# Kernel optimization log

Measured on AMD Instinct MI355X. Metric: run time of the kernel, lower is better.

The kernel has to match this reference:

```python
import jax, jax.numpy as jnp
import numpy as np

N_SAMPLES = 32768
N_FRAMES = 128
MODEL_DIM = 128
N_HARM = 64
N_EVENTS = 8
NYQ = 22050.0 / 2.0
MIN_F = 30.0 / NYQ
MAX_F = 3000.0 / NYQ
SPAN = MAX_F - MIN_F
PI = float(np.pi)


def linterp(x, size):
    # F.interpolate(mode='linear', align_corners=False) along last axis
    n_in = x.shape[-1]
    scale = n_in / size
    coords = (jnp.arange(size, dtype=jnp.float32) + 0.5) * scale - 0.5
    coords = jnp.clip(coords, 0.0, n_in - 1)
    lo = jnp.floor(coords).astype(jnp.int32)
    hi = jnp.minimum(lo + 1, n_in - 1)
    w = coords - lo.astype(jnp.float32)
    return x[..., lo] * (1.0 - w) + x[..., hi] * w


def gumbel_hard(logits, u):
    # F.gumbel_softmax(hard=True), straight-through, tau=1, last axis
    g = -jnp.log(-jnp.log(u + 1e-10) + 1e-10)
    y = jax.nn.softmax(logits + g, axis=-1)
    hard = jax.nn.one_hot(jnp.argmax(y, axis=-1), logits.shape[-1], dtype=y.dtype)
    return hard + y - jax.lax.stop_gradient(y)


def max_norm(x):
    return x / (jnp.max(jnp.abs(x), axis=-1, keepdims=True) + 1e-8)


def fft_convolve(a, b):
    sa = jnp.fft.rfft(a, axis=-1)
    sb = jnp.fft.rfft(b, axis=-1)
    return jnp.fft.irfft(sa * sb, n=a.shape[-1], axis=-1)


def setup_inputs() -> dict:
    key = jax.random.key(0)
    ks = jax.random.split(key, 16)
    B = 4 * N_EVENTS  # 32 flattened event vectors
    s = 0.1  # weight_init
    return {
        "x": jax.random.normal(ks[0], (B, MODEL_DIM), jnp.float32),
        "W_sw": jax.random.normal(ks[1], (MODEL_DIM, 2), jnp.float32) * s,
        "b_sw": jnp.zeros((2,), jnp.float32),
        "W_f0": jax.random.normal(ks[2], (MODEL_DIM, 1), jnp.float32) * s,
        "b_f0": jnp.zeros((1,), jnp.float32),
        "W_fv": jax.random.normal(ks[3], (MODEL_DIM, N_FRAMES), jnp.float32) * s,
        "b_fv": jnp.zeros((N_FRAMES,), jnp.float32),
        "W_amp": jax.random.normal(ks[4], (MODEL_DIM, 2 * N_HARM * N_FRAMES), jnp.float32) * s,
        "b_amp": jnp.zeros((2 * N_HARM * N_FRAMES,), jnp.float32),
        "W_loc": jax.random.normal(ks[5], (MODEL_DIM, N_FRAMES), jnp.float32) * s,
        "b_loc": jnp.zeros((N_FRAMES,), jnp.float32),
        "u_sw": jax.random.uniform(ks[6], (B, 2), jnp.float32),
        "u_loc": jax.random.uniform(ks[7], (B, 1, N_FRAMES), jnp.float32),
        "noise_u": jax.random.uniform(ks[8], (B, 1, N_SAMPLES), jnp.float32),
    }


def reference(x, W_sw, b_sw, W_f0, b_f0, W_fv, b_fv, W_amp, b_amp, W_loc, b_loc, u_sw, u_loc, noise_u):
    B = x.shape[0]
    # switch gate (gumbel hard), keep first channel
    sw = gumbel_hard(x @ W_sw + b_sw, u_sw)[..., :1]  # [B,1]
    # discrete location logits -> gumbel hard one-hot over 128 frames
    disc = jax.nn.sigmoid((x @ W_loc + b_loc).reshape(B, 1, N_FRAMES))
    loc = gumbel_hard(disc, u_loc).reshape(-1, N_EVENTS, N_FRAMES)  # [G,8,128]
    f0 = jax.nn.sigmoid(x @ W_f0 + b_f0) ** 2  # [B,1]
    f0_var = jax.nn.sigmoid((x @ W_fv + b_fv).reshape(B, 1, N_FRAMES)) * 2.0 - 1.0
    amp = ((x @ W_amp + b_amp).reshape(B, 2 * N_HARM, N_FRAMES)) ** 2
    # scatter one-hot locations onto full-rate timeline with stride
    step = N_SAMPLES // N_FRAMES
    loc_full = jnp.zeros((B // N_EVENTS, N_EVENTS, N_SAMPLES), x.dtype).at[:, :, ::step].set(loc)
    f0 = MIN_F + f0 * SPAN
    f0_span = f0 * 0.01
    f0t = f0.reshape(B, 1, 1) + f0_var * f0_span.reshape(B, 1, 1)  # [B,1,128]
    harmonics = jnp.arange(1, N_HARM + 1, dtype=x.dtype)
    harm = f0t * harmonics[None, :, None]  # [B,64,128]
    harm = jnp.where(harm > 1.0, 0.0, harm) * PI  # zero aliased harmonics
    harm = linterp(harm, N_SAMPLES)  # [B,64,N]
    harm = jnp.sin(jnp.cumsum(harm, axis=-1))  # phase-accumulated oscillators
    # noise shaped by 128-tap windowed slice of each oscillator
    noise = noise_u * 2.0 - 1.0  # uniform(-1,1), [B,1,N]
    hw = 0.54 - 0.46 * jnp.cos(2.0 * PI * jnp.arange(128, dtype=x.dtype) / 128.0)
    nf = harm[..., :128] * hw[None, None, :]
    nf = jnp.pad(nf, ((0, 0), (0, 0), (0, N_SAMPLES - 128)))
    nb = jnp.fft.irfft(jnp.fft.rfft(noise, axis=-1, norm='ortho') * jnp.fft.rfft(nf, axis=-1, norm='ortho'), n=N_SAMPLES, axis=-1, norm='ortho')
    nb = max_norm(nb)
    full = jnp.concatenate([harm, nb], axis=1)  # [B,128,N]
    amp = linterp(amp, N_SAMPLES)  # [B,128,N]
    out = full * amp * sw[..., None]
    out = out.reshape(-1, N_EVENTS, 2 * N_HARM, N_SAMPLES).sum(axis=2)  # [G,8,N]
    return fft_convolve(out, loc_full)
```

## Files before the change

### kernel.cpp

```cpp
#include <hip/hip_runtime.h>
#include <math.h>

typedef __attribute__((ext_vector_type(8))) short short8v;
typedef __attribute__((ext_vector_type(4))) float f32x4;

namespace {
constexpr int NSAMP = 32768;
constexpr int NMASK = NSAMP - 1;
constexpr float MIN_F_F = (float)(30.0 / 11025.0);
constexpr float SPAN_F  = (float)(3000.0 / 11025.0 - 30.0 / 11025.0);
constexpr float PI_F    = 3.14159265358979323846f;
constexpr double TWO_PI  = 6.283185307179586476925287;
constexpr double INV_2PI = 0.159154943091895335768884;
constexpr float INV_2PI_F = 0.15915494309189533577f;
constexpr float INV_SQRT_N = 0.00552427172801990295f;

constexpr size_t OFF_PM = 0;
constexpr size_t OFF_V  = OFF_PM + 32*64*128*4;
constexpr size_t OFF_TA = OFF_V  + 32*64*128*4;
constexpr size_t OFF_A  = OFF_TA + 32*64*128*2;
constexpr size_t OFF_M  = OFF_A  + 32*128*128*4;
constexpr size_t OFF_SW = OFF_M  + 2048*4;
constexpr size_t OFF_SH = OFF_SW + 32*4;
constexpr size_t OFF_NM = OFF_SH + 32*4;
}

__device__ __forceinline__ float sigmoidf_(float z) { return 1.0f / (1.0f + expf(-z)); }
__device__ __forceinline__ float gumbelf_(float u) { return -logf(-logf(u + 1e-10f) + 1e-10f); }
__device__ __forceinline__ unsigned short f2bf(float f) {
    unsigned u = __float_as_uint(f);
    return (unsigned short)((u + 0x7FFFu + ((u >> 16) & 1u)) >> 16);
}
__device__ __forceinline__ float sinrev(float r) {
#if __has_builtin(__builtin_amdgcn_sinf)
    return __builtin_amdgcn_sinf(r);
#else
    return __sinf(r * 6.2831853071795864769f);
#endif
}

__launch_bounds__(256)
__global__ void setup_kernel(const float* __restrict__ x,
                             const float* __restrict__ Wsw, const float* __restrict__ bsw,
                             const float* __restrict__ Wf0, const float* __restrict__ bf0,
                             const float* __restrict__ Wfv, const float* __restrict__ bfv,
                             const float* __restrict__ Wamp, const float* __restrict__ bamp,
                             const float* __restrict__ Wloc, const float* __restrict__ bloc,
                             const float* __restrict__ usw, const float* __restrict__ uloc,
                             float* __restrict__ ampT,
                             float* __restrict__ PmodR, float* __restrict__ vfreq,
                             unsigned short* __restrict__ tapsA, float* __restrict__ swb,
                             int* __restrict__ shiftb, unsigned int* __restrict__ maxb,
                             int* __restrict__ nmtb) {
    int tid = threadIdx.x;
    __shared__ float xs[128], f0t[128];
    __shared__ float redA[128]; __shared__ int redI[128];
    __shared__ float red0[128], red1[128], red2[128];
    __shared__ int maxHsh;

    if (blockIdx.x < 256) {
        int bq = blockIdx.x >> 6;
        int jt = blockIdx.x & 63;
        int j = jt * 256 + tid;
        float acc[8];
        float bj = bamp[j];
#pragma unroll
        for (int b = 0; b < 8; ++b) acc[b] = bj;
        const float* xb = x + bq * 8 * 128;
#pragma unroll 8
        for (int d = 0; d < 128; ++d) {
            float wv = Wamp[(size_t)d * 16384 + j];
#pragma unroll
            for (int b = 0; b < 8; ++b) acc[b] = fmaf(xb[b * 128 + d], wv, acc[b]);
        }
        int ch = j >> 7, fr = j & 127;
#pragma unroll
        for (int b = 0; b < 8; ++b) {
            float a = acc[b];
            ampT[(size_t)(bq * 8 + b) * 16384 + fr * 128 + ch] = a * a;
        }
        return;
    }

    int b = blockIdx.x - 256;
    if (tid < 64) maxb[b * 64 + tid] = 0u;
    if (tid == 0) maxHsh = 0;
    if (tid < 128) xs[tid] = x[b * 128 + tid];
    __syncthreads();

    {
        int half = tid >> 7, fr = tid & 127;
        const float* W = half ? Wloc : Wfv;
        float a = (half ? bloc : bfv)[fr];
        for (int d = 0; d < 128; ++d) a = fmaf(xs[d], W[d * 128 + fr], a);
        if (half) { redA[fr] = sigmoidf_(a) + gumbelf_(uloc[b * 128 + fr]); redI[fr] = fr; }
        else      { f0t[fr] = sigmoidf_(a) * 2.0f - 1.0f; }
    }
    if (tid < 128) {
        red0[tid] = xs[tid] * Wsw[tid * 2 + 0];
        red1[tid] = xs[tid] * Wsw[tid * 2 + 1];
        red2[tid] = xs[tid] * Wf0[tid];
    }
    __syncthreads();
    for (int off = 64; off > 0; off >>= 1) {
        if (tid < off) {
            red0[tid] += red0[tid + off];
            red1[tid] += red1[tid + off];
            red2[tid] += red2[tid + off];
            if (redA[tid + off] > redA[tid]) { redA[tid] = redA[tid + off]; redI[tid] = redI[tid + off]; }
        }
        __syncthreads();
    }
    float l0 = red0[0] + bsw[0], l1 = red1[0] + bsw[1];
    float g0 = gumbelf_(usw[b * 2 + 0]), g1 = gumbelf_(usw[b * 2 + 1]);
    float swv = (l0 + g0 >= l1 + g1) ? 1.0f : 0.0f;
    float sg = sigmoidf_(red2[0] + bf0[0]);
    float f0v = MIN_F_F + (sg * sg) * SPAN_F;
    if (tid == 0) { swb[b] = swv; shiftb[b] = redI[0] * 256; }
    if (tid < 128) {
        float f0var = f0t[tid];
        f0t[tid] = f0v + f0var * (f0v * 0.01f);
    }
    __syncthreads();

    int wave = tid >> 6, lane = tid & 63;
    int k0 = lane * 2, k1 = k0 + 1;
    int myMaxH = 0;
    for (int h = wave; h < 64; h += 4) {
        float hf = (float)(h + 1);
        size_t base = ((size_t)b * 64 + h) * 128;
        float vA = f0t[k0] * hf; vA = (vA > 1.0f) ? 0.0f : vA * PI_F;
        float vB = f0t[k1] * hf; vB = (vB > 1.0f) ? 0.0f : vB * PI_F;
        if (__any((vA > 0.0f) || (vB > 0.0f))) myMaxH = h;
        double v0d = (double)vA, v1d = (double)vB;
        double sc = v0d + v1d;
#pragma unroll
        for (int d = 1; d < 64; d <<= 1) {
            double o = __shfl_up(sc, d);
            if (lane >= d) sc += o;
        }
        double P0 = 128.0 * (2.0 * sc - 2.0 * v1d - v0d);
        double P1 = 128.0 * (2.0 * sc - v1d);
        double r0 = P0 * INV_2PI; r0 -= floor(r0);
        double r1 = P1 * INV_2PI; r1 -= floor(r1);
        PmodR[base + k0] = (float)r0;
        PmodR[base + k1] = (float)r1;
        vfreq[base + k0] = vA * INV_2PI_F;
        vfreq[base + k1] = vB * INV_2PI_F;
        float v0_rad = __shfl(vA, 0);
        double v0rev = (double)v0_rad * INV_2PI;
#pragma unroll
        for (int kk = 0; kk < 2; ++kk) {
            int k = k0 + kk;
            float hwk = 0.54f - 0.46f * cosf(6.2831853071795864769f * (float)k / 128.0f);
            double rv = (double)(k + 1) * v0rev; rv -= floor(rv);
            float sv = __sinf((float)(rv * TWO_PI));
            float tv = sv * hwk * INV_SQRT_N;
            int c = k >> 3, e = 7 - (k & 7);
            tapsA[base + 8 * (c ^ (h & 7)) + e] = f2bf(tv);
        }
    }
    if (lane == 0) atomicMax(&maxHsh, myMaxH);
    __syncthreads();
    if (tid == 0) nmtb[b] = (maxHsh >> 4) + 1;
}


template<int NMT>
__device__ __forceinline__ void convmax_core(int tid, const short* tapsL,
                                             const short (*wsh)[640],
                                             unsigned int* maxL) {
    int lane = tid & 63, w = tid >> 6;
    int g = lane >> 4, col = lane & 15, s_l = lane & 7, b3 = (lane >> 3) & 1;
    short8v fa[NMT][4];
#pragma unroll
    for (int mt = 0; mt < NMT; ++mt)
#pragma unroll
        for (int ks = 0; ks < 4; ++ks) {
            int row = 16 * mt + col;
            int ch = (4 * ks + g) ^ (row & 7);
            fa[mt][ks] = *(const short8v*)&tapsL[row * 128 + 8 * ch];
        }
    float rm[NMT * 4];
#pragma unroll
    for (int i = 0; i < NMT * 4; ++i) rm[i] = 0.0f;
    for (int ntl = 0; ntl < 8; ++ntl) {
        int nt = w * 8 + ntl;
        short8v fb[4];
#pragma unroll
        for (int ks = 0; ks < 4; ++ks) {
            int t0 = 120 + 16 * nt - 32 * ks - 8 * g + 8 * b3;
            int ch = (t0 >> 3) ^ s_l;
            fb[ks] = *(const short8v*)&wsh[s_l][8 * ch];
        }
        f32x4 acc[NMT];
#pragma unroll
        for (int mt = 0; mt < NMT; ++mt) acc[mt] = (f32x4){0, 0, 0, 0};
#pragma unroll
        for (int ks = 0; ks < 4; ++ks)
#pragma unroll
            for (int mt = 0; mt < NMT; ++mt)
                acc[mt] = __builtin_amdgcn_mfma_f32_16x16x32_bf16(fa[mt][ks], fb[ks], acc[mt], 0, 0, 0);
#pragma unroll
        for (int mt = 0; mt < NMT; ++mt)
#pragma unroll
            for (int q = 0; q < 4; ++q) rm[mt * 4 + q] = fmaxf(rm[mt * 4 + q], fabsf(acc[mt][q]));
    }
#pragma unroll
    for (int i = 0; i < NMT * 4; ++i) {
        float m = rm[i];
        m = fmaxf(m, __shfl_xor(m, 1));
        m = fmaxf(m, __shfl_xor(m, 2));
        m = fmaxf(m, __shfl_xor(m, 4));
        m = fmaxf(m, __shfl_xor(m, 8));
        if (col == 0) atomicMax(&maxL[16 * (i >> 2) + 4 * g + (i & 3)], __float_as_uint(m));
    }
}

__launch_bounds__(256)
__global__ void convmax_kernel(const float* __restrict__ noise,
                               const unsigned short* __restrict__ tapsA,
                               const float* __restrict__ swb,
                               const int* __restrict__ nmtb,
                               unsigned int* __restrict__ maxb) {
    int b = blockIdx.y;
    if (swb[b] == 0.0f) return;
    int nmt = nmtb[b];
    int tid = threadIdx.x;
    int T = blockIdx.x * 512;
    __shared__ short tapsL[64 * 128];
    __shared__ short wsh[8][640];
    __shared__ float wf[640];
    __shared__ unsigned maxL[64];
    if (tid < 64) maxL[tid] = 0u;
    {
        const short8v* src = (const short8v*)(tapsA + ((size_t)b << 13));
        short8v* dst = (short8v*)tapsL;
        for (int i = tid; i < 1024; i += 256) dst[i] = src[i];
    }
    for (int i = tid; i < 640; i += 256)
        wf[i] = noise[(size_t)b * NSAMP + ((T - 127 + i) & NMASK)] * 2.0f - 1.0f;
    __syncthreads();
    for (int idx = tid; idx < 640; idx += 256) {
        int c = idx >> 3, s = idx & 7;
        short8v v;
#pragma unroll
        for (int e = 0; e < 8; ++e) {
            int t = 8 * c + e + s; t = t < 640 ? t : 639;
            v[e] = (short)f2bf(wf[t]);
        }
        *(short8v*)&wsh[s][8 * (c ^ s)] = v;
    }
    __syncthreads();
    switch (nmt) {
        case 1: convmax_core<1>(tid, tapsL, wsh, maxL); break;
        case 2: convmax_core<2>(tid, tapsL, wsh, maxL); break;
        case 3: convmax_core<3>(tid, tapsL, wsh, maxL); break;
        default: convmax_core<4>(tid, tapsL, wsh, maxL); break;
    }
    __syncthreads();
    if (tid < 64 && tid < nmt * 16) atomicMax(&maxb[b * 64 + tid], maxL[tid]);
}

template<int NMT>
__device__ __forceinline__ void final_core(int b, int T, int tid, int s0, int shift,
                                           const short* tapsL, const short (*wsh)[640],
                                           const float4 (*seg)[64],
                                           const float (*ampA)[64], const float (*ampBn)[64],
                                           float (*part)[520], float* __restrict__ out) {
    int lane = tid & 63, w = tid >> 6;
    int g = lane >> 4, col = lane & 15, s_l = lane & 7, b3 = (lane >> 3) & 1;
    short8v fa[NMT][4];
#pragma unroll
    for (int mt = 0; mt < NMT; ++mt)
#pragma unroll
        for (int ks = 0; ks < 4; ++ks) {
            int row = 16 * mt + col;
            int ch = (4 * ks + g) ^ (row & 7);
            fa[mt][ks] = *(const short8v*)&tapsL[row * 128 + 8 * ch];
        }
    int dd = (w + 1) >> 1;
    bool head = (T + w * 128) < 128;
    float vsr[NMT * 4], dvr[NMT * 4], pbr[NMT * 4];
#pragma unroll
    for (int mt = 0; mt < NMT; ++mt)
#pragma unroll
        for (int q = 0; q < 4; ++q) {
            int i = mt * 4 + q, h = 16 * mt + 4 * g + q;
            float4 sgv = seg[dd][h];
            vsr[i] = sgv.x;
            dvr[i] = head ? 0.0f : sgv.y;
            pbr[i] = head ? (-128.0f * sgv.x) : sgv.z;
        }
    int t_0 = T + w * 128 + col;
    int lo0 = (t_0 < 128) ? 0 : ((t_0 - 128) >> 8);
    int dlo = lo0 - s0;
    float loF = (float)lo0;
    f32x4 aloA[NMT], adA[NMT], aloB[NMT], adB[NMT];
#pragma unroll
    for (int mt = 0; mt < NMT; ++mt) {
        int h4 = 16 * mt + 4 * g;
        aloA[mt] = *(const f32x4*)&ampA[dlo][h4];
        adA[mt]  = *(const f32x4*)&ampA[dlo + 1][h4] - aloA[mt];
        aloB[mt] = *(const f32x4*)&ampBn[dlo][h4];
        adB[mt]  = *(const f32x4*)&ampBn[dlo + 1][h4] - aloB[mt];
    }
    __syncthreads();

    for (int ntl = 0; ntl < 8; ++ntl) {
        int nt = w * 8 + ntl;
        short8v fb[4];
#pragma unroll
        for (int ks = 0; ks < 4; ++ks) {
            int t0 = 120 + 16 * nt - 32 * ks - 8 * g + 8 * b3;
            int ch = (t0 >> 3) ^ s_l;
            fb[ks] = *(const short8v*)&wsh[s_l][8 * ch];
        }
        f32x4 acc[NMT];
#pragma unroll
        for (int mt = 0; mt < NMT; ++mt) acc[mt] = (f32x4){0, 0, 0, 0};
#pragma unroll
        for (int ks = 0; ks < 4; ++ks)
#pragma unroll
            for (int mt = 0; mt < NMT; ++mt)
                acc[mt] = __builtin_amdgcn_mfma_f32_16x16x32_bf16(fa[mt][ks], fb[ks], acc[mt], 0, 0, 0);

        int j = w * 128 + ntl * 16 + col;
        int t = T + j;
        float coords = ((float)t + 0.5f) * (1.0f / 256.0f) - 0.5f;
        coords = fminf(fmaxf(coords, 0.0f), 127.0f);
        float w1 = coords - loF;
        float mp1 = (float)(((t - 128) & 255) + 1);
        float mp2 = mp1 * mp1;
        float psum = 0.0f;
#pragma unroll
        for (int mt = 0; mt < NMT; ++mt) {
#pragma unroll
            for (int q = 0; q < 4; ++q) {
                int i = mt * 4 + q;
                float p = fmaf(mp2, dvr[i], fmaf(mp1, vsr[i], pbr[i]));
                p -= floorf(p);
                float sv = sinrev(p);
                float aA = fmaf(w1, adA[mt][q], aloA[mt][q]);
                float aB = fmaf(w1, adB[mt][q], aloB[mt][q]);
                psum = fmaf(sv, aA, psum);
                psum = fmaf(acc[mt][q], aB, psum);
            }
        }
        part[g][j] = psum;
    }
    __syncthreads();
#pragma unroll
    for (int rep = 0; rep < 2; ++rep) {
        int j2 = rep * 256 + tid;
        float r = part[0][j2] + part[1][j2] + part[2][j2] + part[3][j2];
        int pos = (T + j2 + shift) & NMASK;
        out[(size_t)b * NSAMP + pos] = r;
    }
}

__launch_bounds__(256)
__global__ void final_kernel(const float* __restrict__ noise,
                             const unsigned short* __restrict__ tapsA,
                             const float* __restrict__ PmodR, const float* __restrict__ vfreq,
                             const float* __restrict__ ampT,
                             const unsigned int* __restrict__ maxb,
                             const float* __restrict__ swb, const int* __restrict__ shiftb,
                             const int* __restrict__ nmtb,
                             float* __restrict__ out) {
    int b = blockIdx.y;
    int T = blockIdx.x * 512, tid = threadIdx.x;
    if (swb[b] == 0.0f) {
        out[(size_t)b * NSAMP + T + tid] = 0.0f;
        out[(size_t)b * NSAMP + T + 256 + tid] = 0.0f;
        return;
    }
    int nmt = nmtb[b];
    __shared__ union { short tapsL[64 * 128]; float part[4][520]; } R;
    __shared__ short wsh[8][640];
    __shared__ float wf[640];
    __shared__ float4 seg[3][64];
    __shared__ float ampA[4][64], ampBn[4][64];

    int s0 = (T >> 8) - 1;
    for (int i = tid; i < 640; i += 256)
        wf[i] = noise[(size_t)b * NSAMP + ((T - 127 + i) & NMASK)] * 2.0f - 1.0f;
    {
        const short8v* src = (const short8v*)(tapsA + ((size_t)b << 13));
        short8v* dst = (short8v*)R.tapsL;
        for (int i = tid; i < 1024; i += 256) dst[i] = src[i];
    }
    {
        int ad = tid >> 6, ah = tid & 63;
        int afr = min(max(s0 + ad, 0), 127);
        float aAv = ampT[(size_t)b * 16384 + afr * 128 + ah];
        float aBv = ampT[(size_t)b * 16384 + afr * 128 + 64 + ah];
        float invn = 1.0f / (__uint_as_float(maxb[b * 64 + ah]) + 1e-8f);
        ampA[ad][ah] = aAv;
        ampBn[ad][ah] = aBv * invn;
    }
    if (tid < 192) {
        int dd = tid >> 6, h2 = tid & 63;
        size_t vb = ((size_t)(b * 64 + h2)) * 128;
        int s = min(max(s0 + dd, 0), 127), s1 = min(s + 1, 127);
        float vs = vfreq[vb + s], vs1 = vfreq[vb + s1];
        float4 sgv;
        sgv.x = vs;
        sgv.y = (vs1 - vs) * (1.0f / 512.0f);
        sgv.z = PmodR[vb + s];
        sgv.w = 0.0f;
        seg[dd][h2] = sgv;
    }
    __syncthreads();
    for (int idx = tid; idx < 640; idx += 256) {
        int c = idx >> 3, s = idx & 7;
        short8v v;
#pragma unroll
        for (int e = 0; e < 8; ++e) {
            int t = 8 * c + e + s; t = t < 640 ? t : 639;
            v[e] = (short)f2bf(wf[t]);
        }
        *(short8v*)&wsh[s][8 * (c ^ s)] = v;
    }
    int shift = shiftb[b];
    switch (nmt) {
        case 1: final_core<1>(b, T, tid, s0, shift, R.tapsL, wsh, seg, ampA, ampBn, R.part, out); break;
        case 2: final_core<2>(b, T, tid, s0, shift, R.tapsL, wsh, seg, ampA, ampBn, R.part, out); break;
        case 3: final_core<3>(b, T, tid, s0, shift, R.tapsL, wsh, seg, ampA, ampBn, R.part, out); break;
        default: final_core<4>(b, T, tid, s0, shift, R.tapsL, wsh, seg, ampA, ampBn, R.part, out); break;
    }
}

extern "C" void kernel_launch(void* const* d_in, const int* in_sizes, int n_in,
                              void* d_out, int out_size, void* d_ws, size_t ws_size,
                              hipStream_t stream) {
    const float* x     = (const float*)d_in[0];
    const float* Wsw   = (const float*)d_in[1];
    const float* bsw   = (const float*)d_in[2];
    const float* Wf0   = (const float*)d_in[3];
    const float* bf0   = (const float*)d_in[4];
    const float* Wfv   = (const float*)d_in[5];
    const float* bfv   = (const float*)d_in[6];
    const float* Wamp  = (const float*)d_in[7];
    const float* bamp  = (const float*)d_in[8];
    const float* Wloc  = (const float*)d_in[9];
    const float* bloc  = (const float*)d_in[10];
    const float* usw   = (const float*)d_in[11];
    const float* uloc  = (const float*)d_in[12];
    const float* noise = (const float*)d_in[13];

    char* ws = (char*)d_ws;
    float*    PmodR  = (float*)(ws + OFF_PM);
    float*    vfreq  = (float*)(ws + OFF_V);
    unsigned short* tapsA = (unsigned short*)(ws + OFF_TA);
    float*    ampT   = (float*)(ws + OFF_A);
    unsigned* maxb   = (unsigned*)(ws + OFF_M);
    float*    swb    = (float*)(ws + OFF_SW);
    int*      shiftb = (int*)(ws + OFF_SH);
    int*      nmtb   = (int*)(ws + OFF_NM);
    float*    out    = (float*)d_out;

    setup_kernel<<<dim3(288), 256, 0, stream>>>(x, Wsw, bsw, Wf0, bf0, Wfv, bfv, Wamp, bamp,
                                                Wloc, bloc, usw, uloc, ampT,
                                                PmodR, vfreq, tapsA, swb, shiftb, maxb, nmtb);
    convmax_kernel<<<dim3(64, 32), 256, 0, stream>>>(noise, tapsA, swb, nmtb, maxb);
    final_kernel<<<dim3(64, 32), 256, 0, stream>>>(noise, tapsA, PmodR, vfreq, ampT, maxb,
                                                   swb, shiftb, nmtb, out);
}
```

Baseline: 49.92 us.

## Move amp GEMM into conv-max kernel and reduce final partials via shuffles

The amplitude projection GEMM moves out of the setup kernel into the conv-max launch as extra blocks. The short per-event prep kernel (32 blocks) now finishes sooner, and the heavy GEMM runs alongside the convolution-max blocks. In the final kernel, the cross-group partial-sum reduction through shared memory and two barriers is replaced by wave shuffles, and each lane writes its output directly. This removes the shared union buffer and a barrier, at the cost of narrower 16-lane global stores.

```diff
diff --git a/kernel.cpp b/kernel.cpp
--- a/kernel.cpp
+++ b/kernel.cpp
@@ -40,49 +40,23 @@
 }
 
 __launch_bounds__(256)
-__global__ void setup_kernel(const float* __restrict__ x,
-                             const float* __restrict__ Wsw, const float* __restrict__ bsw,
-                             const float* __restrict__ Wf0, const float* __restrict__ bf0,
-                             const float* __restrict__ Wfv, const float* __restrict__ bfv,
-                             const float* __restrict__ Wamp, const float* __restrict__ bamp,
-                             const float* __restrict__ Wloc, const float* __restrict__ bloc,
-                             const float* __restrict__ usw, const float* __restrict__ uloc,
-                             float* __restrict__ ampT,
-                             float* __restrict__ PmodR, float* __restrict__ vfreq,
-                             unsigned short* __restrict__ tapsA, float* __restrict__ swb,
-                             int* __restrict__ shiftb, unsigned int* __restrict__ maxb,
-                             int* __restrict__ nmtb) {
+__global__ void prep_kernel(const float* __restrict__ x,
+                            const float* __restrict__ Wsw, const float* __restrict__ bsw,
+                            const float* __restrict__ Wf0, const float* __restrict__ bf0,
+                            const float* __restrict__ Wfv, const float* __restrict__ bfv,
+                            const float* __restrict__ Wloc, const float* __restrict__ bloc,
+                            const float* __restrict__ usw, const float* __restrict__ uloc,
+                            float* __restrict__ PmodR, float* __restrict__ vfreq,
+                            unsigned short* __restrict__ tapsA, float* __restrict__ swb,
+                            int* __restrict__ shiftb, unsigned int* __restrict__ maxb,
+                            int* __restrict__ nmtb) {
     int tid = threadIdx.x;
     __shared__ float xs[128], f0t[128];
     __shared__ float redA[128]; __shared__ int redI[128];
     __shared__ float red0[128], red1[128], red2[128];
     __shared__ int maxHsh;
 
-    if (blockIdx.x < 256) {
-        int bq = blockIdx.x >> 6;
-        int jt = blockIdx.x & 63;
-        int j = jt * 256 + tid;
-        float acc[8];
-        float bj = bamp[j];
-#pragma unroll
-        for (int b = 0; b < 8; ++b) acc[b] = bj;
-        const float* xb = x + bq * 8 * 128;
-#pragma unroll 8
-        for (int d = 0; d < 128; ++d) {
-            float wv = Wamp[(size_t)d * 16384 + j];
-#pragma unroll
-            for (int b = 0; b < 8; ++b) acc[b] = fmaf(xb[b * 128 + d], wv, acc[b]);
-        }
-        int ch = j >> 7, fr = j & 127;
-#pragma unroll
-        for (int b = 0; b < 8; ++b) {
-            float a = acc[b];
-            ampT[(size_t)(bq * 8 + b) * 16384 + fr * 128 + ch] = a * a;
-        }
-        return;
-    }
-
-    int b = blockIdx.x - 256;
+    int b = blockIdx.x;
     if (tid < 64) maxb[b * 64 + tid] = 0u;
     if (tid == 0) maxHsh = 0;
     if (tid < 128) xs[tid] = x[b * 128 + tid];
@@ -218,20 +192,49 @@
 }
 
 __launch_bounds__(256)
-__global__ void convmax_kernel(const float* __restrict__ noise,
+__global__ void ampconv_kernel(const float* __restrict__ x,
+                               const float* __restrict__ Wamp, const float* __restrict__ bamp,
+                               float* __restrict__ ampT,
+                               const float* __restrict__ noise,
                                const unsigned short* __restrict__ tapsA,
                                const float* __restrict__ swb,
                                const int* __restrict__ nmtb,
                                unsigned int* __restrict__ maxb) {
-    int b = blockIdx.y;
-    if (swb[b] == 0.0f) return;
-    int nmt = nmtb[b];
     int tid = threadIdx.x;
-    int T = blockIdx.x * 512;
     __shared__ short tapsL[64 * 128];
     __shared__ short wsh[8][640];
     __shared__ float wf[640];
     __shared__ unsigned maxL[64];
+
+    if (blockIdx.x < 256) {
+        int bq = blockIdx.x >> 6;
+        int jt = blockIdx.x & 63;
+        int j = jt * 256 + tid;
+        float acc[8];
+        float bj = bamp[j];
+#pragma unroll
+        for (int b = 0; b < 8; ++b) acc[b] = bj;
+        const float* xb = x + bq * 8 * 128;
+#pragma unroll 8
+        for (int d = 0; d < 128; ++d) {
+            float wv = Wamp[(size_t)d * 16384 + j];
+#pragma unroll
+            for (int b = 0; b < 8; ++b) acc[b] = fmaf(xb[b * 128 + d], wv, acc[b]);
+        }
+        int ch = j >> 7, fr = j & 127;
+#pragma unroll
+        for (int b = 0; b < 8; ++b) {
+            float a = acc[b];
+            ampT[(size_t)(bq * 8 + b) * 16384 + fr * 128 + ch] = a * a;
+        }
+        return;
+    }
+
+    int bx = blockIdx.x - 256;
+    int b = bx >> 6;
+    if (swb[b] == 0.0f) return;
+    int nmt = nmtb[b];
+    int T = (bx & 63) * 512;
     if (tid < 64) maxL[tid] = 0u;
     {
         const short8v* src = (const short8v*)(tapsA + ((size_t)b << 13));
@@ -267,7 +270,7 @@
                                            const short* tapsL, const short (*wsh)[640],
                                            const float4 (*seg)[64],
                                            const float (*ampA)[64], const float (*ampBn)[64],
-                                           float (*part)[520], float* __restrict__ out) {
+                                           float* __restrict__ out) {
     int lane = tid & 63, w = tid >> 6;
     int g = lane >> 4, col = lane & 15, s_l = lane & 7, b3 = (lane >> 3) & 1;
     short8v fa[NMT][4];
@@ -305,7 +308,6 @@
         aloB[mt] = *(const f32x4*)&ampBn[dlo][h4];
         adB[mt]  = *(const f32x4*)&ampBn[dlo + 1][h4] - aloB[mt];
     }
-    __syncthreads();
 
     for (int ntl = 0; ntl < 8; ++ntl) {
         int nt = w * 8 + ntl;
@@ -347,15 +349,12 @@
                 psum = fmaf(acc[mt][q], aB, psum);
             }
         }
-        part[g][j] = psum;
-    }
-    __syncthreads();
-#pragma unroll
-    for (int rep = 0; rep < 2; ++rep) {
-        int j2 = rep * 256 + tid;
-        float r = part[0][j2] + part[1][j2] + part[2][j2] + part[3][j2];
-        int pos = (T + j2 + shift) & NMASK;
-        out[(size_t)b * NSAMP + pos] = r;
+        psum += __shfl_xor(psum, 16);
+        psum += __shfl_xor(psum, 32);
+        if (lane < 16) {
+            int pos = (T + j + shift) & NMASK;
+            out[(size_t)b * NSAMP + pos] = psum;
+        }
     }
 }
 
@@ -376,7 +375,7 @@
         return;
     }
     int nmt = nmtb[b];
-    __shared__ union { short tapsL[64 * 128]; float part[4][520]; } R;
+    __shared__ short tapsL[64 * 128];
     __shared__ short wsh[8][640];
     __shared__ float wf[640];
     __shared__ float4 seg[3][64];
@@ -387,7 +386,7 @@
         wf[i] = noise[(size_t)b * NSAMP + ((T - 127 + i) & NMASK)] * 2.0f - 1.0f;
     {
         const short8v* src = (const short8v*)(tapsA + ((size_t)b << 13));
-        short8v* dst = (short8v*)R.tapsL;
+        short8v* dst = (short8v*)tapsL;
         for (int i = tid; i < 1024; i += 256) dst[i] = src[i];
     }
     {
@@ -422,12 +421,13 @@
         }
         *(short8v*)&wsh[s][8 * (c ^ s)] = v;
     }
+    __syncthreads();
     int shift = shiftb[b];
     switch (nmt) {
-        case 1: final_core<1>(b, T, tid, s0, shift, R.tapsL, wsh, seg, ampA, ampBn, R.part, out); break;
-        case 2: final_core<2>(b, T, tid, s0, shift, R.tapsL, wsh, seg, ampA, ampBn, R.part, out); break;
-        case 3: final_core<3>(b, T, tid, s0, shift, R.tapsL, wsh, seg, ampA, ampBn, R.part, out); break;
-        default: final_core<4>(b, T, tid, s0, shift, R.tapsL, wsh, seg, ampA, ampBn, R.part, out); break;
+        case 1: final_core<1>(b, T, tid, s0, shift, tapsL, wsh, seg, ampA, ampBn, out); break;
+        case 2: final_core<2>(b, T, tid, s0, shift, tapsL, wsh, seg, ampA, ampBn, out); break;
+        case 3: final_core<3>(b, T, tid, s0, shift, tapsL, wsh, seg, ampA, ampBn, out); break;
+        default: final_core<4>(b, T, tid, s0, shift, tapsL, wsh, seg, ampA, ampBn, out); break;
     }
 }
 
@@ -460,10 +460,11 @@
     int*      nmtb   = (int*)(ws + OFF_NM);
     float*    out    = (float*)d_out;
 
-    setup_kernel<<<dim3(288), 256, 0, stream>>>(x, Wsw, bsw, Wf0, bf0, Wfv, bfv, Wamp, bamp,
-                                                Wloc, bloc, usw, uloc, ampT,
-                                                PmodR, vfreq, tapsA, swb, shiftb, maxb, nmtb);
-    convmax_kernel<<<dim3(64, 32), 256, 0, stream>>>(noise, tapsA, swb, nmtb, maxb);
+    prep_kernel<<<dim3(32), 256, 0, stream>>>(x, Wsw, bsw, Wf0, bf0, Wfv, bfv, Wloc, bloc,
+                                              usw, uloc, PmodR, vfreq, tapsA, swb, shiftb,
+                                              maxb, nmtb);
+    ampconv_kernel<<<dim3(2304), 256, 0, stream>>>(x, Wamp, bamp, ampT, noise, tapsA,
+                                                   swb, nmtb, maxb);
     final_kernel<<<dim3(64, 32), 256, 0, stream>>>(noise, tapsA, PmodR, vfreq, ampT, maxb,
                                                    swb, shiftb, nmtb, out);
 }
```

Measured after the change: 54.40 us. 9.0% more time.
